# Kernel tuning notes

Hardware: AMD Instinct MI355X
Metric: run time of the kernel (lower is better)

The kernel has to match this reference:

```python
import jax, jax.numpy as jnp
import numpy as np

N_NODES = 50000
N_EDGES = 800000
C = 128
NEG_SLOPE = 0.01  # nn.LeakyReLU default


def _init_linear(key, fan_in, fan_out):
    kw, kb = jax.random.split(key)
    lim = 1.0 / np.sqrt(fan_in)
    W = jax.random.uniform(kw, (fan_in, fan_out), jnp.float32, -lim, lim)
    b = jax.random.uniform(kb, (fan_out,), jnp.float32, -lim, lim)
    return W, b


def setup_inputs() -> dict:
    key = jax.random.key(0)
    ks = jax.random.split(key, 10)
    x = jax.random.normal(ks[0], (N_NODES, C), jnp.float32)
    pos = jax.random.normal(ks[1], (N_NODES, 3), jnp.float32)
    edge_index = jax.random.randint(ks[2], (2, N_EDGES), 0, N_NODES, jnp.int64)
    # mlp_h: Linear(C,C) -> LeakyReLU -> Linear(C,3) -> Tanh
    Wh1, bh1 = _init_linear(ks[3], C, C)
    Wh2, bh2 = _init_linear(ks[4], C, 3)
    # mlp_f: Linear(C+3, C) -> LeakyReLU
    Wf, bf = _init_linear(ks[5], C + 3, C)
    # mlp_g: Linear(C,C) -> LeakyReLU -> Linear(C,C)
    Wg1, bg1 = _init_linear(ks[6], C, C)
    Wg2, bg2 = _init_linear(ks[7], C, C)
    return {"x": x, "pos": pos, "edge_index": edge_index,
            "Wh1": Wh1, "bh1": bh1, "Wh2": Wh2, "bh2": bh2,
            "Wf": Wf, "bf": bf,
            "Wg1": Wg1, "bg1": bg1, "Wg2": Wg2, "bg2": bg2}


def reference(x, pos, edge_index, Wh1, bh1, Wh2, bh2, Wf, bf, Wg1, bg1, Wg2, bg2):
    lrelu = lambda t: jax.nn.leaky_relu(t, NEG_SLOPE)
    # delta_i = tanh(mlp_h(x_i))  -> [N, 3]
    delta = jnp.tanh(lrelu(x @ Wh1 + bh1) @ Wh2 + bh2)
    src, dst = edge_index[0], edge_index[1]  # message j -> i (PyG convention)
    # per-edge relative position: pos_j - pos_i + delta_i  -> [E, 3]
    rel = pos[src] - pos[dst] + delta[dst]
    # per-edge message: mlp_f([rel, x_j])  -> [E, C]
    e = lrelu(jnp.concatenate([rel, x[src]], axis=-1) @ Wf + bf)
    # scatter-max aggregate over incoming edges per target node
    agg = jax.ops.segment_max(e, dst, num_segments=N_NODES)
    agg = jnp.where(jnp.isfinite(agg), agg, 0.0)  # empty segments -> 0
    # out_i = mlp_g(agg_i) + x_i
    out = lrelu(agg @ Wg1 + bg1) @ Wg2 + bg2 + x
    return out
```

## Files before the change

### kernel.cpp

```cpp
#include <hip/hip_runtime.h>
#include <cfloat>
#include <cmath>

#define NEG_SLOPE 0.01f

typedef __attribute__((ext_vector_type(8))) short short8;
typedef __attribute__((ext_vector_type(4))) float f32x4;

__device__ __forceinline__ float lrelu(float v) { return v >= 0.0f ? v : NEG_SLOPE * v; }

__device__ __forceinline__ ushort f2b(float f) {
    unsigned u = __float_as_uint(f);
    u += 0x7fffu + ((u >> 16) & 1u);
    return (ushort)(u >> 16);
}
__device__ __forceinline__ float b2f(ushort s) { return __uint_as_float(((unsigned)s) << 16); }

__device__ __forceinline__ void split8(const float* v, short8& hi, short8& lo) {
#pragma unroll
    for (int j = 0; j < 8; ++j) {
        ushort h = f2b(v[j]);
        hi[j] = (short)h;
        lo[j] = (short)f2b(v[j] - b2f(h));
    }
}

__global__ __launch_bounds__(256) void wprep_kernel(
    const float* __restrict__ Wh1, const float* __restrict__ Wf,
    const float* __restrict__ Wg1, const float* __restrict__ Wg2,
    ushort* __restrict__ WT)
{
    int tt = blockIdx.x * 256 + threadIdx.x;
    int mat = tt >> 14;
    int idx = tt & 16383;
    int n = idx >> 7, k = idx & 127;
    float v;
    if (mat == 0)      v = Wh1[k * 128 + n];
    else if (mat == 1) v = Wf[(k + 3) * 128 + n];
    else if (mat == 2) v = Wg1[k * 128 + n];
    else               v = Wg2[k * 128 + n];
    WT[(tt - idx) + n * 128 + k] = f2b(v);
}

__global__ __launch_bounds__(256) void scanA_kernel(
    const int* __restrict__ G, int* __restrict__ partial)
{
    __shared__ int s[256];
    int i = blockIdx.x * 256 + threadIdx.x;
    s[threadIdx.x] = G[i];
    __syncthreads();
    for (int d = 128; d > 0; d >>= 1) {
        if (threadIdx.x < d) s[threadIdx.x] += s[threadIdx.x + d];
        __syncthreads();
    }
    if (threadIdx.x == 0) partial[blockIdx.x] = s[0];
}

__global__ __launch_bounds__(256) void scanBC_kernel(
    int* __restrict__ G, const int* __restrict__ partial, int NB)
{
    __shared__ int s[256];
    __shared__ int base;
    const int t = threadIdx.x;
    int v = (t < NB) ? partial[t] : 0;
    s[t] = v;
    __syncthreads();
    for (int d = 1; d < 256; d <<= 1) {
        int a = (t >= d) ? s[t - d] : 0;
        __syncthreads();
        s[t] += a;
        __syncthreads();
    }
    if (t == blockIdx.x) base = s[t] - v;
    __syncthreads();

    int i = blockIdx.x * 256 + t;
    int g = G[i];
    s[t] = g;
    __syncthreads();
    for (int d = 1; d < 256; d <<= 1) {
        int a = (t >= d) ? s[t - d] : 0;
        __syncthreads();
        s[t] += a;
        __syncthreads();
    }
    G[i] = base + s[t] - g;
}

__global__ __launch_bounds__(256) void partition_kernel(
    const int* __restrict__ ei, const int* __restrict__ G,
    uint* __restrict__ bpairs, int E, int NBK)
{
    __shared__ int cur[256];
    const int tid = threadIdx.x;
    if (tid < NBK) cur[tid] = G[tid * 256 + blockIdx.x];
    __syncthreads();
    for (int e = blockIdx.x * 256 + tid; e < E; e += 65536) {
        int src = ei[e];
        int dst = ei[E + e];
        int p = atomicAdd(&cur[dst >> 8], 1);
        bpairs[p] = (uint)src | ((uint)(dst & 255) << 24);
    }
}

__global__ __launch_bounds__(256) void bucket_csr_kernel(
    const uint* __restrict__ bpairs, const int* __restrict__ G,
    int* __restrict__ offs, int* __restrict__ srcs, int E, int M, int NBK)
{
    __shared__ int deg[256], scn[256], cur[256];
    const int b = blockIdx.x;
    const int t = threadIdx.x;
    const int base = G[b * 256];
    const int end  = (b + 1 < NBK) ? G[(b + 1) * 256] : E;
    deg[t] = 0;
    __syncthreads();
    for (int p = base + t; p < end; p += 256)
        atomicAdd(&deg[bpairs[p] >> 24], 1);
    __syncthreads();
    scn[t] = deg[t];
    __syncthreads();
    for (int d = 1; d < 256; d <<= 1) {
        int a = (t >= d) ? scn[t - d] : 0;
        __syncthreads();
        scn[t] += a;
        __syncthreads();
    }
    int excl = scn[t] - deg[t];
    cur[t] = excl;
    int node = b * 256 + t;
    if (node < M) offs[node] = base + excl;
    if (node == M - 1 || (b == NBK - 1 && t == 255)) offs[M] = E;
    __syncthreads();
    for (int p = base + t; p < end; p += 256) {
        uint pk = bpairs[p];
        int qpos = atomicAdd(&cur[pk >> 24], 1);
        srcs[base + qpos] = (int)(pk & 0xFFFFFFu);
    }
}


#define GEMM_CORE_REG(ACC, AH, AL)                                              \
    {                                                                           \
        _Pragma("unroll")                                                       \
        for (int ks = 0; ks < 4; ++ks) {                                        \
            _Pragma("unroll")                                                   \
            for (int nt = 0; nt < 8; ++nt) {                                    \
                short8 bfr = *(const short8*)&Bs[(nt * 16 + ln) * 136 + ks * 32 + qd * 8]; \
                ACC[nt] = __builtin_amdgcn_mfma_f32_16x16x32_bf16(AL[ks], bfr, ACC[nt], 0, 0, 0); \
                ACC[nt] = __builtin_amdgcn_mfma_f32_16x16x32_bf16(AH[ks], bfr, ACC[nt], 0, 0, 0); \
            }                                                                   \
        }                                                                       \
    }

#define STAGE_B(WTP)                                                            \
    {                                                                           \
        _Pragma("unroll")                                                       \
        for (int i = 0; i < 8; ++i) {                                           \
            int c = tid + 256 * i;                                              \
            int r = c >> 4, col8 = (c & 15) * 8;                                \
            *(uint4*)&Bs[r * 136 + col8] = *(const uint4*)((WTP) + r * 128 + col8); \
        }                                                                       \
    }

__global__ __launch_bounds__(256) void fused_count_hy_kernel(
    const int* __restrict__ ei, int* __restrict__ G, int E, int NBK,
    const float* __restrict__ x, const ushort* __restrict__ WT,
    const float* __restrict__ bh1, const float* __restrict__ Wh2,
    const float* __restrict__ bh2, const float* __restrict__ Wf,
    const float* __restrict__ pos, float* __restrict__ q,
    ushort* __restrict__ yb, int M)
{
    __shared__ ushort Bs[128 * 136];
    __shared__ ushort yS[64 * 128];
    const int tid = threadIdx.x;

    if (blockIdx.x < 256) {
        int* cnt = (int*)yS;
        const int b = blockIdx.x;
        cnt[tid] = 0;
        __syncthreads();
        for (int e = b * 256 + tid; e < E; e += 65536)
            atomicAdd(&cnt[ei[E + e] >> 8], 1);
        __syncthreads();
        if (tid < NBK) G[tid * 256 + b] = cnt[tid];
        return;
    }

    const int w = tid >> 6, L = tid & 63, qd = L >> 4, ln = L & 15;
    const int row0 = (blockIdx.x - 256) * 64;
    const int arow = row0 + w * 16 + ln;

    short8 ah[4], al[4];
    {
        const float* base = x + (size_t)((arow < M) ? arow : 0) * 128 + qd * 8;
        float vb[8];
#pragma unroll
        for (int ks = 0; ks < 4; ++ks) {
            float4 v0 = make_float4(0.f, 0.f, 0.f, 0.f), v1 = v0;
            if (arow < M) {
                v0 = *(const float4*)(base + ks * 32);
                v1 = *(const float4*)(base + ks * 32 + 4);
            }
            vb[0] = v0.x; vb[1] = v0.y; vb[2] = v0.z; vb[3] = v0.w;
            vb[4] = v1.x; vb[5] = v1.y; vb[6] = v1.z; vb[7] = v1.w;
            split8(vb, ah[ks], al[ks]);
        }
    }

    STAGE_B(WT);
    __syncthreads();
    f32x4 acc1[8];
#pragma unroll
    for (int nt = 0; nt < 8; ++nt) acc1[nt] = (f32x4){0.f, 0.f, 0.f, 0.f};
    GEMM_CORE_REG(acc1, ah, al);
    __syncthreads();

    STAGE_B(WT + 16384);
    __syncthreads();
    f32x4 acc2[8];
#pragma unroll
    for (int nt = 0; nt < 8; ++nt) acc2[nt] = (f32x4){0.f, 0.f, 0.f, 0.f};
    GEMM_CORE_REG(acc2, ah, al);
    __syncthreads();

    float* h1s = (float*)Bs;
#pragma unroll
    for (int nt = 0; nt < 8; ++nt) {
        int n = nt * 16 + ln;
        float bias = bh1[n];
#pragma unroll
        for (int r = 0; r < 4; ++r)
            h1s[(w * 16 + qd * 4 + r) * 132 + n] = lrelu(acc1[nt][r] + bias);
    }
#pragma unroll
    for (int r = 0; r < 4; ++r) {
        int m = w * 16 + qd * 4 + r;
        int gm = row0 + m;
        float p0 = 0.f, p1 = 0.f, p2 = 0.f;
        if (gm < M) { p0 = pos[gm * 3]; p1 = pos[gm * 3 + 1]; p2 = pos[gm * 3 + 2]; }
#pragma unroll
        for (int nt = 0; nt < 8; ++nt) {
            int n = nt * 16 + ln;
            yS[m * 128 + n] = f2b(acc2[nt][r] + p0 * Wf[n] + p1 * Wf[128 + n] + p2 * Wf[256 + n]);
        }
    }
    __syncthreads();

    int row = tid & 63, cc = tid >> 6;
    if (cc < 3 && row0 + row < M) {
        float s = 0.f;
#pragma unroll
        for (int k4 = 0; k4 < 32; ++k4) {
            float4 h = *(const float4*)&h1s[row * 132 + k4 * 4];
            s += h.x * Wh2[(k4 * 4 + 0) * 3 + cc] + h.y * Wh2[(k4 * 4 + 1) * 3 + cc]
               + h.z * Wh2[(k4 * 4 + 2) * 3 + cc] + h.w * Wh2[(k4 * 4 + 3) * 3 + cc];
        }
        q[(row0 + row) * 3 + cc] = tanhf(s + bh2[cc]) - pos[(row0 + row) * 3 + cc];
    }
#pragma unroll
    for (int i = 0; i < 4; ++i) {
        int c = tid + 256 * i;
        int r = c >> 4, col8 = (c & 15) * 8;
        if (row0 + r < M)
            *(uint4*)(yb + (size_t)(row0 + r) * 128 + col8) = *(const uint4*)&yS[r * 128 + col8];
    }
}

__global__ __launch_bounds__(256) void agg_kernel(
    const int* __restrict__ offs, const int* __restrict__ srcs,
    const ushort* __restrict__ yb, ushort* __restrict__ aggb, int M)
{
    int wave = threadIdx.x >> 6;
    int lane = threadIdx.x & 63;
    int node = blockIdx.x * 4 + wave;
    if (node >= M) return;
    int o0 = offs[node], o1 = offs[node + 1];
    float a0 = -INFINITY, a1 = -INFINITY;
    const uint* yp = (const uint*)yb;
    int j = o0;
    for (; j + 7 < o1; j += 8) {
        uint u[8];
#pragma unroll
        for (int t = 0; t < 8; ++t)
            u[t] = yp[(size_t)srcs[j + t] * 64 + lane];
#pragma unroll
        for (int t = 0; t < 8; ++t) {
            a0 = fmaxf(a0, __uint_as_float(u[t] << 16));
            a1 = fmaxf(a1, __uint_as_float(u[t] & 0xFFFF0000u));
        }
    }
    for (; j + 3 < o1; j += 4) {
        uint u[4];
#pragma unroll
        for (int t = 0; t < 4; ++t)
            u[t] = yp[(size_t)srcs[j + t] * 64 + lane];
#pragma unroll
        for (int t = 0; t < 4; ++t) {
            a0 = fmaxf(a0, __uint_as_float(u[t] << 16));
            a1 = fmaxf(a1, __uint_as_float(u[t] & 0xFFFF0000u));
        }
    }
    for (; j < o1; ++j) {
        uint u = yp[(size_t)srcs[j] * 64 + lane];
        a0 = fmaxf(a0, __uint_as_float(u << 16));
        a1 = fmaxf(a1, __uint_as_float(u & 0xFFFF0000u));
    }
    uint pk = (__float_as_uint(a0) >> 16) | (__float_as_uint(a1) & 0xFFFF0000u);
    ((uint*)aggb)[(size_t)node * 64 + lane] = pk;
}

__global__ __launch_bounds__(256) void midout_kernel(
    const ushort* __restrict__ aggb, const float* __restrict__ qv,
    const float* __restrict__ Wf, const float* __restrict__ bfv,
    const ushort* __restrict__ Wg1T, const float* __restrict__ bg1,
    const ushort* __restrict__ Wg2T, const float* __restrict__ bg2,
    const float* __restrict__ x, float* __restrict__ out, int M)
{
    __shared__ ushort Bs[128 * 136];
    __shared__ ushort Ms[64 * 136];
    const int tid = threadIdx.x;
    const int w = tid >> 6, L = tid & 63, qd = L >> 4, ln = L & 15;
    const int row0 = blockIdx.x * 64;
    const int arow = row0 + w * 16 + ln;

    short8 ah[4], al[4];
    {
        bool ok = arow < M;
        const ushort* base = aggb + (size_t)(ok ? arow : 0) * 128 + qd * 8;
        float q0 = 0.f, q1 = 0.f, q2 = 0.f;
        if (ok) { q0 = qv[arow * 3]; q1 = qv[arow * 3 + 1]; q2 = qv[arow * 3 + 2]; }
        float vb[8];
#pragma unroll
        for (int ks = 0; ks < 4; ++ks) {
            union { uint4 u; ushort s[8]; } a;
            a.u = ok ? *(const uint4*)(base + ks * 32) : make_uint4(0xFF80FF80u, 0xFF80FF80u, 0xFF80FF80u, 0xFF80FF80u);
#pragma unroll
            for (int j = 0; j < 8; ++j) {
                int k = ks * 32 + qd * 8 + j;
                float dec = 0.f;
                if (a.s[j] != 0xFF80u)
                    dec = lrelu(b2f(a.s[j]) + q0 * Wf[k] + q1 * Wf[128 + k] + q2 * Wf[256 + k] + bfv[k]);
                vb[j] = dec;
            }
            split8(vb, ah[ks], al[ks]);
        }
    }

    STAGE_B(Wg1T);
    __syncthreads();
    f32x4 macc[8];
#pragma unroll
    for (int nt = 0; nt < 8; ++nt) macc[nt] = (f32x4){0.f, 0.f, 0.f, 0.f};
    GEMM_CORE_REG(macc, ah, al);
    __syncthreads();

#pragma unroll
    for (int nt = 0; nt < 8; ++nt) {
        int n = nt * 16 + ln;
        float bias = bg1[n];
#pragma unroll
        for (int r = 0; r < 4; ++r)
            Ms[(w * 16 + qd * 4 + r) * 136 + n] = f2b(lrelu(macc[nt][r] + bias));
    }
    STAGE_B(Wg2T);
    __syncthreads();

    short8 a2[4];
#pragma unroll
    for (int ks = 0; ks < 4; ++ks)
        a2[ks] = *(const short8*)&Ms[(w * 16 + ln) * 136 + ks * 32 + qd * 8];

    f32x4 acc2[8];
#pragma unroll
    for (int nt = 0; nt < 8; ++nt) acc2[nt] = (f32x4){0.f, 0.f, 0.f, 0.f};
#pragma unroll
    for (int ks = 0; ks < 4; ++ks) {
#pragma unroll
        for (int nt = 0; nt < 8; ++nt) {
            short8 bfr = *(const short8*)&Bs[(nt * 16 + ln) * 136 + ks * 32 + qd * 8];
            acc2[nt] = __builtin_amdgcn_mfma_f32_16x16x32_bf16(a2[ks], bfr, acc2[nt], 0, 0, 0);
        }
    }
    __syncthreads();

    float* outS = (float*)Bs;
#pragma unroll
    for (int r = 0; r < 4; ++r) {
        int m = w * 16 + qd * 4 + r;
#pragma unroll
        for (int nt = 0; nt < 8; ++nt)
            outS[m * 132 + nt * 16 + ln] = acc2[nt][r];
    }
    __syncthreads();
#pragma unroll
    for (int i = 0; i < 8; ++i) {
        int c = tid + 256 * i;
        int r = c >> 5, col4 = (c & 31) * 4;
        int gr = row0 + r;
        if (gr < M) {
            float4 o = *(const float4*)&outS[r * 132 + col4];
            float4 bv = *(const float4*)(bg2 + col4);
            float4 xv = *(const float4*)(x + (size_t)gr * 128 + col4);
            o.x += bv.x + xv.x; o.y += bv.y + xv.y;
            o.z += bv.z + xv.z; o.w += bv.w + xv.w;
            *(float4*)(out + (size_t)gr * 128 + col4) = o;
        }
    }
}

extern "C" void kernel_launch(void* const* d_in, const int* in_sizes, int n_in,
                              void* d_out, int out_size, void* d_ws, size_t ws_size,
                              hipStream_t stream)
{
    const float* x   = (const float*)d_in[0];
    const float* pos = (const float*)d_in[1];
    const int*   ei  = (const int*)d_in[2];
    const float* Wh1 = (const float*)d_in[3];
    const float* bh1 = (const float*)d_in[4];
    const float* Wh2 = (const float*)d_in[5];
    const float* bh2 = (const float*)d_in[6];
    const float* Wf  = (const float*)d_in[7];
    const float* bf  = (const float*)d_in[8];
    const float* Wg1 = (const float*)d_in[9];
    const float* bg1 = (const float*)d_in[10];
    const float* Wg2 = (const float*)d_in[11];
    const float* bg2 = (const float*)d_in[12];
    float* out = (float*)d_out;

    const int M = in_sizes[0] / 128;
    const int E = in_sizes[2] / 2;
    const int NBK = (M + 255) >> 8;

    char* ws = (char*)d_ws;
    size_t off = 0;
    auto alloc = [&](size_t bytes) { void* p = ws + off; off += (bytes + 255) & ~255ull; return p; };
    ushort* yb     = (ushort*)alloc((size_t)M * 128 * sizeof(ushort));
    ushort* aggb   = (ushort*)alloc((size_t)M * 128 * sizeof(ushort));
    ushort* WT     = (ushort*)alloc(4 * 16384 * sizeof(ushort));
    float*  q      = (float*)alloc((size_t)M * 3 * sizeof(float));
    int*    offs   = (int*)alloc((size_t)(M + 1) * sizeof(int));
    int*    G      = (int*)alloc((size_t)NBK * 256 * sizeof(int));
    int*    part   = (int*)alloc(256 * sizeof(int));
    uint*   bpairs = (uint*)alloc((size_t)E * sizeof(uint));
    int*    srcs   = (int*)alloc((size_t)E * sizeof(int));

    const int gb = (M + 63) / 64;

    wprep_kernel<<<256, 256, 0, stream>>>(Wh1, Wf, Wg1, Wg2, WT);
    fused_count_hy_kernel<<<256 + gb, 256, 0, stream>>>(
        ei, G, E, NBK, x, WT, bh1, Wh2, bh2, Wf, pos, q, yb, M);
    scanA_kernel<<<NBK, 256, 0, stream>>>(G, part);
    scanBC_kernel<<<NBK, 256, 0, stream>>>(G, part, NBK);
    partition_kernel<<<256, 256, 0, stream>>>(ei, G, bpairs, E, NBK);
    bucket_csr_kernel<<<NBK, 256, 0, stream>>>(bpairs, G, offs, srcs, E, M, NBK);
    agg_kernel<<<(M + 3) / 4, 256, 0, stream>>>(offs, srcs, yb, aggb, M);
    midout_kernel<<<gb, 256, 0, stream>>>(aggb, q, Wf, bf,
                                          WT + 2 * 16384, bg1,
                                          WT + 3 * 16384, bg2, x, out, M);
}
```

Measured before the change: 208.0 us.

## Replace two-level bucketed CSR build with direct global-atomic degree count and placement

Replaces the bucketed counting sort (per-bucket LDS histograms, two-kernel scan, partition into packed pairs, per-bucket CSR) with per-node global atomic degree counts, a single scan kernel and a direct atomic placement of source indices. This cuts two kernel launches and the intermediate bpairs round trip through memory. In exchange it relies on scattered global atomics over 50k counters and on each scan block re-summing all preceding degree blocks. Edge order within each node's list becomes nondeterministic, which does not affect a max aggregation.

After: 286.0 us. 1.38x slower.

```diff
diff --git a/kernel.cpp b/kernel.cpp
--- a/kernel.cpp
+++ b/kernel.cpp
@@ -28,9 +28,10 @@
 __global__ __launch_bounds__(256) void wprep_kernel(
     const float* __restrict__ Wh1, const float* __restrict__ Wf,
     const float* __restrict__ Wg1, const float* __restrict__ Wg2,
-    ushort* __restrict__ WT)
+    ushort* __restrict__ WT, int* __restrict__ deg, int NDEG)
 {
     int tt = blockIdx.x * 256 + threadIdx.x;
+    if (tt < NDEG) deg[tt] = 0;
     int mat = tt >> 14;
     int idx = tt & 16383;
     int n = idx >> 7, k = idx & 127;
@@ -42,28 +43,24 @@
     WT[(tt - idx) + n * 128 + k] = f2b(v);
 }
 
-__global__ __launch_bounds__(256) void scanA_kernel(
-    const int* __restrict__ G, int* __restrict__ partial)
+__global__ __launch_bounds__(256) void scan_kernel(
+    const int* __restrict__ deg, int* __restrict__ offs, int* __restrict__ cur,
+    int M, int E)
 {
     __shared__ int s[256];
-    int i = blockIdx.x * 256 + threadIdx.x;
-    s[threadIdx.x] = G[i];
+    const int b = blockIdx.x, t = threadIdx.x;
+    int part = 0;
+    for (int k = 0; k < b; ++k) part += deg[k * 256 + t];
+    s[t] = part;
     __syncthreads();
     for (int d = 128; d > 0; d >>= 1) {
-        if (threadIdx.x < d) s[threadIdx.x] += s[threadIdx.x + d];
+        if (t < d) s[t] += s[t + d];
         __syncthreads();
     }
-    if (threadIdx.x == 0) partial[blockIdx.x] = s[0];
-}
-
-__global__ __launch_bounds__(256) void scanBC_kernel(
-    int* __restrict__ G, const int* __restrict__ partial, int NB)
-{
-    __shared__ int s[256];
-    __shared__ int base;
-    const int t = threadIdx.x;
-    int v = (t < NB) ? partial[t] : 0;
-    s[t] = v;
+    int base = s[0];
+    __syncthreads();
+    int dv = deg[b * 256 + t];
+    s[t] = dv;
     __syncthreads();
     for (int d = 1; d < 256; d <<= 1) {
         int a = (t >= d) ? s[t - d] : 0;
@@ -71,70 +68,21 @@
         s[t] += a;
         __syncthreads();
     }
-    if (t == blockIdx.x) base = s[t] - v;
-    __syncthreads();
-
-    int i = blockIdx.x * 256 + t;
-    int g = G[i];
-    s[t] = g;
-    __syncthreads();
-    for (int d = 1; d < 256; d <<= 1) {
-        int a = (t >= d) ? s[t - d] : 0;
-        __syncthreads();
-        s[t] += a;
-        __syncthreads();
-    }
-    G[i] = base + s[t] - g;
-}
-
-__global__ __launch_bounds__(256) void partition_kernel(
-    const int* __restrict__ ei, const int* __restrict__ G,
-    uint* __restrict__ bpairs, int E, int NBK)
-{
-    __shared__ int cur[256];
-    const int tid = threadIdx.x;
-    if (tid < NBK) cur[tid] = G[tid * 256 + blockIdx.x];
-    __syncthreads();
-    for (int e = blockIdx.x * 256 + tid; e < E; e += 65536) {
+    int node = b * 256 + t;
+    int off = base + s[t] - dv;
+    if (node < M) { offs[node] = off; cur[node] = off; }
+    if (node == M - 1) offs[M] = off + dv;
+}
+
+__global__ __launch_bounds__(256) void place_kernel(
+    const int* __restrict__ ei, int* __restrict__ cur,
+    int* __restrict__ srcs, int E)
+{
+    for (int e = blockIdx.x * 256 + threadIdx.x; e < E; e += 262144) {
         int src = ei[e];
         int dst = ei[E + e];
-        int p = atomicAdd(&cur[dst >> 8], 1);
-        bpairs[p] = (uint)src | ((uint)(dst & 255) << 24);
-    }
-}
-
-__global__ __launch_bounds__(256) void bucket_csr_kernel(
-    const uint* __restrict__ bpairs, const int* __restrict__ G,
-    int* __restrict__ offs, int* __restrict__ srcs, int E, int M, int NBK)
-{
-    __shared__ int deg[256], scn[256], cur[256];
-    const int b = blockIdx.x;
-    const int t = threadIdx.x;
-    const int base = G[b * 256];
-    const int end  = (b + 1 < NBK) ? G[(b + 1) * 256] : E;
-    deg[t] = 0;
-    __syncthreads();
-    for (int p = base + t; p < end; p += 256)
-        atomicAdd(&deg[bpairs[p] >> 24], 1);
-    __syncthreads();
-    scn[t] = deg[t];
-    __syncthreads();
-    for (int d = 1; d < 256; d <<= 1) {
-        int a = (t >= d) ? scn[t - d] : 0;
-        __syncthreads();
-        scn[t] += a;
-        __syncthreads();
-    }
-    int excl = scn[t] - deg[t];
-    cur[t] = excl;
-    int node = b * 256 + t;
-    if (node < M) offs[node] = base + excl;
-    if (node == M - 1 || (b == NBK - 1 && t == 255)) offs[M] = E;
-    __syncthreads();
-    for (int p = base + t; p < end; p += 256) {
-        uint pk = bpairs[p];
-        int qpos = atomicAdd(&cur[pk >> 24], 1);
-        srcs[base + qpos] = (int)(pk & 0xFFFFFFu);
+        int p = atomicAdd(&cur[dst], 1);
+        srcs[p] = src;
     }
 }
 
@@ -163,7 +111,7 @@
     }
 
 __global__ __launch_bounds__(256) void fused_count_hy_kernel(
-    const int* __restrict__ ei, int* __restrict__ G, int E, int NBK,
+    const int* __restrict__ ei, int* __restrict__ deg, int E,
     const float* __restrict__ x, const ushort* __restrict__ WT,
     const float* __restrict__ bh1, const float* __restrict__ Wh2,
     const float* __restrict__ bh2, const float* __restrict__ Wf,
@@ -175,14 +123,9 @@
     const int tid = threadIdx.x;
 
     if (blockIdx.x < 256) {
-        int* cnt = (int*)yS;
         const int b = blockIdx.x;
-        cnt[tid] = 0;
-        __syncthreads();
         for (int e = b * 256 + tid; e < E; e += 65536)
-            atomicAdd(&cnt[ei[E + e] >> 8], 1);
-        __syncthreads();
-        if (tid < NBK) G[tid * 256 + b] = cnt[tid];
+            atomicAdd(&deg[ei[E + e]], 1);
         return;
     }
 
@@ -430,6 +373,7 @@
     const int M = in_sizes[0] / 128;
     const int E = in_sizes[2] / 2;
     const int NBK = (M + 255) >> 8;
+    const int NDEG = NBK * 256;
 
     char* ws = (char*)d_ws;
     size_t off = 0;
@@ -439,20 +383,17 @@
     ushort* WT     = (ushort*)alloc(4 * 16384 * sizeof(ushort));
     float*  q      = (float*)alloc((size_t)M * 3 * sizeof(float));
     int*    offs   = (int*)alloc((size_t)(M + 1) * sizeof(int));
-    int*    G      = (int*)alloc((size_t)NBK * 256 * sizeof(int));
-    int*    part   = (int*)alloc(256 * sizeof(int));
-    uint*   bpairs = (uint*)alloc((size_t)E * sizeof(uint));
+    int*    deg    = (int*)alloc((size_t)NDEG * sizeof(int));
+    int*    cur    = (int*)alloc((size_t)NDEG * sizeof(int));
     int*    srcs   = (int*)alloc((size_t)E * sizeof(int));
 
     const int gb = (M + 63) / 64;
 
-    wprep_kernel<<<256, 256, 0, stream>>>(Wh1, Wf, Wg1, Wg2, WT);
+    wprep_kernel<<<256, 256, 0, stream>>>(Wh1, Wf, Wg1, Wg2, WT, deg, NDEG);
     fused_count_hy_kernel<<<256 + gb, 256, 0, stream>>>(
-        ei, G, E, NBK, x, WT, bh1, Wh2, bh2, Wf, pos, q, yb, M);
-    scanA_kernel<<<NBK, 256, 0, stream>>>(G, part);
-    scanBC_kernel<<<NBK, 256, 0, stream>>>(G, part, NBK);
-    partition_kernel<<<256, 256, 0, stream>>>(ei, G, bpairs, E, NBK);
-    bucket_csr_kernel<<<NBK, 256, 0, stream>>>(bpairs, G, offs, srcs, E, M, NBK);
+        ei, deg, E, x, WT, bh1, Wh2, bh2, Wf, pos, q, yb, M);
+    scan_kernel<<<NBK, 256, 0, stream>>>(deg, offs, cur, M, E);
+    place_kernel<<<1024, 256, 0, stream>>>(ei, cur, srcs, E);
     agg_kernel<<<(M + 3) / 4, 256, 0, stream>>>(offs, srcs, yb, aggb, M);
     midout_kernel<<<gb, 256, 0, stream>>>(aggb, q, Wf, bf,
                                           WT + 2 * 16384, bg1,
```

## Merge scan, partition and bucket CSR kernels into one cooperative kernel

Applied to the files above, without the earlier changes.

Replaces four separate launches (two-level scan, partition, per-bucket CSR build) with one cooperative kernel of 256 blocks that separates the phases with grid-wide syncs. The aim is to remove launch overhead and inter-kernel gaps for these small CSR-construction stages. In exchange it depends on all 256 blocks being co-resident and pays for grid barriers and thread fences, and blocks beyond NBK sit idle in several phases.

Result: slower. 392.6 us (+88.8%).

```diff
diff --git a/kernel.cpp b/kernel.cpp
--- a/kernel.cpp
+++ b/kernel.cpp
@@ -1,6 +1,9 @@
 #include <hip/hip_runtime.h>
+#include <hip/hip_cooperative_groups.h>
 #include <cfloat>
 #include <cmath>
+
+namespace cg = cooperative_groups;
 
 #define NEG_SLOPE 0.01f
 
@@ -42,99 +45,97 @@
     WT[(tt - idx) + n * 128 + k] = f2b(v);
 }
 
-__global__ __launch_bounds__(256) void scanA_kernel(
-    const int* __restrict__ G, int* __restrict__ partial)
-{
-    __shared__ int s[256];
-    int i = blockIdx.x * 256 + threadIdx.x;
-    s[threadIdx.x] = G[i];
-    __syncthreads();
-    for (int d = 128; d > 0; d >>= 1) {
-        if (threadIdx.x < d) s[threadIdx.x] += s[threadIdx.x + d];
-        __syncthreads();
-    }
-    if (threadIdx.x == 0) partial[blockIdx.x] = s[0];
-}
-
-__global__ __launch_bounds__(256) void scanBC_kernel(
-    int* __restrict__ G, const int* __restrict__ partial, int NB)
-{
-    __shared__ int s[256];
-    __shared__ int base;
-    const int t = threadIdx.x;
-    int v = (t < NB) ? partial[t] : 0;
-    s[t] = v;
-    __syncthreads();
-    for (int d = 1; d < 256; d <<= 1) {
-        int a = (t >= d) ? s[t - d] : 0;
-        __syncthreads();
-        s[t] += a;
-        __syncthreads();
-    }
-    if (t == blockIdx.x) base = s[t] - v;
-    __syncthreads();
-
-    int i = blockIdx.x * 256 + t;
-    int g = G[i];
-    s[t] = g;
-    __syncthreads();
-    for (int d = 1; d < 256; d <<= 1) {
-        int a = (t >= d) ? s[t - d] : 0;
-        __syncthreads();
-        s[t] += a;
-        __syncthreads();
-    }
-    G[i] = base + s[t] - g;
-}
-
-__global__ __launch_bounds__(256) void partition_kernel(
-    const int* __restrict__ ei, const int* __restrict__ G,
-    uint* __restrict__ bpairs, int E, int NBK)
-{
-    __shared__ int cur[256];
-    const int tid = threadIdx.x;
-    if (tid < NBK) cur[tid] = G[tid * 256 + blockIdx.x];
-    __syncthreads();
-    for (int e = blockIdx.x * 256 + tid; e < E; e += 65536) {
-        int src = ei[e];
-        int dst = ei[E + e];
-        int p = atomicAdd(&cur[dst >> 8], 1);
-        bpairs[p] = (uint)src | ((uint)(dst & 255) << 24);
-    }
-}
-
-__global__ __launch_bounds__(256) void bucket_csr_kernel(
-    const uint* __restrict__ bpairs, const int* __restrict__ G,
-    int* __restrict__ offs, int* __restrict__ srcs, int E, int M, int NBK)
-{
-    __shared__ int deg[256], scn[256], cur[256];
+__global__ __launch_bounds__(256) void build_kernel(
+    const int* __restrict__ ei, int* __restrict__ G, int* __restrict__ part,
+    uint* __restrict__ bpairs, int* __restrict__ offs, int* __restrict__ srcs,
+    int E, int M, int NBK)
+{
+    cg::grid_group grid = cg::this_grid();
     const int b = blockIdx.x;
     const int t = threadIdx.x;
-    const int base = G[b * 256];
-    const int end  = (b + 1 < NBK) ? G[(b + 1) * 256] : E;
-    deg[t] = 0;
-    __syncthreads();
-    for (int p = base + t; p < end; p += 256)
-        atomicAdd(&deg[bpairs[p] >> 24], 1);
-    __syncthreads();
-    scn[t] = deg[t];
-    __syncthreads();
-    for (int d = 1; d < 256; d <<= 1) {
-        int a = (t >= d) ? scn[t - d] : 0;
-        __syncthreads();
-        scn[t] += a;
-        __syncthreads();
-    }
-    int excl = scn[t] - deg[t];
-    cur[t] = excl;
-    int node = b * 256 + t;
-    if (node < M) offs[node] = base + excl;
-    if (node == M - 1 || (b == NBK - 1 && t == 255)) offs[M] = E;
-    __syncthreads();
-    for (int p = base + t; p < end; p += 256) {
-        uint pk = bpairs[p];
-        int qpos = atomicAdd(&cur[pk >> 24], 1);
-        srcs[base + qpos] = (int)(pk & 0xFFFFFFu);
+    __shared__ int s[256], a2[256], a3[256];
+    __shared__ int base_s;
+
+    if (b < NBK) {
+        s[t] = G[b * 256 + t];
+        __syncthreads();
+        for (int d = 128; d > 0; d >>= 1) {
+            if (t < d) s[t] += s[t + d];
+            __syncthreads();
+        }
+        if (t == 0) part[b] = s[0];
+    }
+    __threadfence();
+    grid.sync();
+
+    if (b < NBK) {
+        int v = (t < NBK) ? part[t] : 0;
+        s[t] = v;
+        __syncthreads();
+        for (int d = 1; d < 256; d <<= 1) {
+            int a = (t >= d) ? s[t - d] : 0;
+            __syncthreads();
+            s[t] += a;
+            __syncthreads();
+        }
+        if (t == b) base_s = s[t] - v;
+        __syncthreads();
+
+        int i = b * 256 + t;
+        int g = G[i];
+        s[t] = g;
+        __syncthreads();
+        for (int d = 1; d < 256; d <<= 1) {
+            int a = (t >= d) ? s[t - d] : 0;
+            __syncthreads();
+            s[t] += a;
+            __syncthreads();
+        }
+        G[i] = base_s + s[t] - g;
+    }
+    __threadfence();
+    grid.sync();
+
+    {
+        if (t < NBK) a2[t] = G[t * 256 + b];
+        __syncthreads();
+        for (int e = b * 256 + t; e < E; e += 65536) {
+            int src = ei[e];
+            int dst = ei[E + e];
+            int p = atomicAdd(&a2[dst >> 8], 1);
+            bpairs[p] = (uint)src | ((uint)(dst & 255) << 24);
+        }
+    }
+    __threadfence();
+    grid.sync();
+
+    if (b < NBK) {
+        const int base = G[b * 256];
+        const int end  = (b + 1 < NBK) ? G[(b + 1) * 256] : E;
+        s[t] = 0;
+        __syncthreads();
+        for (int p = base + t; p < end; p += 256)
+            atomicAdd(&s[bpairs[p] >> 24], 1);
+        __syncthreads();
+        a2[t] = s[t];
+        __syncthreads();
+        for (int d = 1; d < 256; d <<= 1) {
+            int a = (t >= d) ? a2[t - d] : 0;
+            __syncthreads();
+            a2[t] += a;
+            __syncthreads();
+        }
+        int excl = a2[t] - s[t];
+        a3[t] = excl;
+        int node = b * 256 + t;
+        if (node < M) offs[node] = base + excl;
+        if (node == M - 1 || (b == NBK - 1 && t == 255)) offs[M] = E;
+        __syncthreads();
+        for (int p = base + t; p < end; p += 256) {
+            uint pk = bpairs[p];
+            int qpos = atomicAdd(&a3[pk >> 24], 1);
+            srcs[base + qpos] = (int)(pk & 0xFFFFFFu);
+        }
     }
 }
 
@@ -449,10 +450,16 @@
     wprep_kernel<<<256, 256, 0, stream>>>(Wh1, Wf, Wg1, Wg2, WT);
     fused_count_hy_kernel<<<256 + gb, 256, 0, stream>>>(
         ei, G, E, NBK, x, WT, bh1, Wh2, bh2, Wf, pos, q, yb, M);
-    scanA_kernel<<<NBK, 256, 0, stream>>>(G, part);
-    scanBC_kernel<<<NBK, 256, 0, stream>>>(G, part, NBK);
-    partition_kernel<<<256, 256, 0, stream>>>(ei, G, bpairs, E, NBK);
-    bucket_csr_kernel<<<NBK, 256, 0, stream>>>(bpairs, G, offs, srcs, E, M, NBK);
+    {
+        const int* ei_a = ei; int* G_a = G; int* part_a = part;
+        uint* bp_a = bpairs; int* offs_a = offs; int* srcs_a = srcs;
+        int E_a = E, M_a = M, NBK_a = NBK;
+        void* args[] = { (void*)&ei_a, (void*)&G_a, (void*)&part_a,
+                         (void*)&bp_a, (void*)&offs_a, (void*)&srcs_a,
+                         (void*)&E_a, (void*)&M_a, (void*)&NBK_a };
+        hipLaunchCooperativeKernel((void*)build_kernel, dim3(256), dim3(256),
+                                   args, 0, stream);
+    }
     agg_kernel<<<(M + 3) / 4, 256, 0, stream>>>(offs, srcs, yb, aggb, M);
     midout_kernel<<<gb, 256, 0, stream>>>(aggb, q, Wf, bf,
                                           WT + 2 * 16384, bg1,
```

## Fuse bucket-count scan into partition kernel, dropping two scan launches

Applied to the files above, without the earlier changes.

The two-level scan over per-block bucket counts (scanA, scanBC) is removed. Each partition block now redundantly reads the full 256x256 count matrix, builds its own column totals and per-block prefix, and scans the bucket totals in shared memory before scattering edges. The count layout is transposed so each block writes one contiguous row. This cuts two kernel launches and their serialization, in exchange for every block re-reading a 256 KB count table.

New measurement: 216.8 us. 1.04x slower.

```diff
diff --git a/kernel.cpp b/kernel.cpp
--- a/kernel.cpp
+++ b/kernel.cpp
@@ -42,28 +42,22 @@
     WT[(tt - idx) + n * 128 + k] = f2b(v);
 }
 
-__global__ __launch_bounds__(256) void scanA_kernel(
-    const int* __restrict__ G, int* __restrict__ partial)
+__global__ __launch_bounds__(256) void scan_partition_kernel(
+    const int* __restrict__ ei, const int* __restrict__ G,
+    int* __restrict__ bbase, uint* __restrict__ bpairs, int E)
 {
     __shared__ int s[256];
-    int i = blockIdx.x * 256 + threadIdx.x;
-    s[threadIdx.x] = G[i];
-    __syncthreads();
-    for (int d = 128; d > 0; d >>= 1) {
-        if (threadIdx.x < d) s[threadIdx.x] += s[threadIdx.x + d];
-        __syncthreads();
-    }
-    if (threadIdx.x == 0) partial[blockIdx.x] = s[0];
-}
-
-__global__ __launch_bounds__(256) void scanBC_kernel(
-    int* __restrict__ G, const int* __restrict__ partial, int NB)
-{
-    __shared__ int s[256];
-    __shared__ int base;
+    __shared__ int cur[256];
+    const int b = blockIdx.x;
     const int t = threadIdx.x;
-    int v = (t < NB) ? partial[t] : 0;
-    s[t] = v;
+
+    int cs = 0, pp = 0;
+    for (int bb = 0; bb < 256; ++bb) {
+        int v = G[bb * 256 + t];
+        if (bb < b) pp += v;
+        cs += v;
+    }
+    s[t] = cs;
     __syncthreads();
     for (int d = 1; d < 256; d <<= 1) {
         int a = (t >= d) ? s[t - d] : 0;
@@ -71,31 +65,15 @@
         s[t] += a;
         __syncthreads();
     }
-    if (t == blockIdx.x) base = s[t] - v;
-    __syncthreads();
-
-    int i = blockIdx.x * 256 + t;
-    int g = G[i];
-    s[t] = g;
-    __syncthreads();
-    for (int d = 1; d < 256; d <<= 1) {
-        int a = (t >= d) ? s[t - d] : 0;
-        __syncthreads();
-        s[t] += a;
-        __syncthreads();
-    }
-    G[i] = base + s[t] - g;
-}
-
-__global__ __launch_bounds__(256) void partition_kernel(
-    const int* __restrict__ ei, const int* __restrict__ G,
-    uint* __restrict__ bpairs, int E, int NBK)
-{
-    __shared__ int cur[256];
-    const int tid = threadIdx.x;
-    if (tid < NBK) cur[tid] = G[tid * 256 + blockIdx.x];
-    __syncthreads();
-    for (int e = blockIdx.x * 256 + tid; e < E; e += 65536) {
+    int colbase = s[t] - cs;
+    cur[t] = colbase + pp;
+    if (b == 0) {
+        bbase[t] = colbase;
+        if (t == 255) bbase[256] = colbase + cs;
+    }
+    __syncthreads();
+
+    for (int e = b * 256 + t; e < E; e += 65536) {
         int src = ei[e];
         int dst = ei[E + e];
         int p = atomicAdd(&cur[dst >> 8], 1);
@@ -104,14 +82,14 @@
 }
 
 __global__ __launch_bounds__(256) void bucket_csr_kernel(
-    const uint* __restrict__ bpairs, const int* __restrict__ G,
+    const uint* __restrict__ bpairs, const int* __restrict__ bbase,
     int* __restrict__ offs, int* __restrict__ srcs, int E, int M, int NBK)
 {
     __shared__ int deg[256], scn[256], cur[256];
     const int b = blockIdx.x;
     const int t = threadIdx.x;
-    const int base = G[b * 256];
-    const int end  = (b + 1 < NBK) ? G[(b + 1) * 256] : E;
+    const int base = bbase[b];
+    const int end  = bbase[b + 1];
     deg[t] = 0;
     __syncthreads();
     for (int p = base + t; p < end; p += 256)
@@ -163,7 +141,7 @@
     }
 
 __global__ __launch_bounds__(256) void fused_count_hy_kernel(
-    const int* __restrict__ ei, int* __restrict__ G, int E, int NBK,
+    const int* __restrict__ ei, int* __restrict__ G, int E,
     const float* __restrict__ x, const ushort* __restrict__ WT,
     const float* __restrict__ bh1, const float* __restrict__ Wh2,
     const float* __restrict__ bh2, const float* __restrict__ Wf,
@@ -182,7 +160,7 @@
         for (int e = b * 256 + tid; e < E; e += 65536)
             atomicAdd(&cnt[ei[E + e] >> 8], 1);
         __syncthreads();
-        if (tid < NBK) G[tid * 256 + b] = cnt[tid];
+        G[b * 256 + tid] = cnt[tid];
         return;
     }
 
@@ -439,8 +417,8 @@
     ushort* WT     = (ushort*)alloc(4 * 16384 * sizeof(ushort));
     float*  q      = (float*)alloc((size_t)M * 3 * sizeof(float));
     int*    offs   = (int*)alloc((size_t)(M + 1) * sizeof(int));
-    int*    G      = (int*)alloc((size_t)NBK * 256 * sizeof(int));
-    int*    part   = (int*)alloc(256 * sizeof(int));
+    int*    G      = (int*)alloc(256 * 256 * sizeof(int));
+    int*    bbase  = (int*)alloc(257 * sizeof(int));
     uint*   bpairs = (uint*)alloc((size_t)E * sizeof(uint));
     int*    srcs   = (int*)alloc((size_t)E * sizeof(int));
 
@@ -448,11 +426,9 @@
 
     wprep_kernel<<<256, 256, 0, stream>>>(Wh1, Wf, Wg1, Wg2, WT);
     fused_count_hy_kernel<<<256 + gb, 256, 0, stream>>>(
-        ei, G, E, NBK, x, WT, bh1, Wh2, bh2, Wf, pos, q, yb, M);
-    scanA_kernel<<<NBK, 256, 0, stream>>>(G, part);
-    scanBC_kernel<<<NBK, 256, 0, stream>>>(G, part, NBK);
-    partition_kernel<<<256, 256, 0, stream>>>(ei, G, bpairs, E, NBK);
-    bucket_csr_kernel<<<NBK, 256, 0, stream>>>(bpairs, G, offs, srcs, E, M, NBK);
+        ei, G, E, x, WT, bh1, Wh2, bh2, Wf, pos, q, yb, M);
+    scan_partition_kernel<<<256, 256, 0, stream>>>(ei, G, bbase, bpairs, E);
+    bucket_csr_kernel<<<NBK, 256, 0, stream>>>(bpairs, bbase, offs, srcs, E, M, NBK);
     agg_kernel<<<(M + 3) / 4, 256, 0, stream>>>(offs, srcs, yb, aggb, M);
     midout_kernel<<<gb, 256, 0, stream>>>(aggb, q, Wf, bf,
                                           WT + 2 * 16384, bg1,
```
